# Kernel optimization log

Hardware: AMD Instinct MI355X
Metric: run time of the kernel (lower is better)

Reference implementation:

```python
import jax, jax.numpy as jnp
import numpy as np

B, N, START = 16, 16, 2048
D, H, HK, DH, CTX = 4096, 32, 8, 128, 4096
T = START + N
REP = H // HK
ROPE_THETA = 500000.0


def setup_inputs() -> dict:
    key = jax.random.key(0)
    ks = jax.random.split(key, 8)
    x = jax.random.normal(ks[0], (B, N, D), jnp.float32)
    # rotary frequencies for absolute positions START..T-1
    half = DH // 2
    inv_freq = 1.0 / (ROPE_THETA ** (np.arange(half, dtype=np.float64) * 2.0 / DH))
    pos = np.arange(START, T, dtype=np.float64)
    ang = pos[:, None] * inv_freq[None, :]  # (N, DH//2)
    freqs_cos = jnp.asarray(np.cos(ang), jnp.float32)
    freqs_sin = jnp.asarray(np.sin(ang), jnp.float32)
    # causal additive mask: query i (abs pos START+i) may attend to key j <= START+i
    i = np.arange(N)[:, None]
    j = np.arange(T)[None, :]
    mask = np.where(j <= START + i, 0.0, -1e9).astype(np.float32)
    mask = jnp.asarray(mask)[None, None]  # (1,1,N,T)
    cache_k = jax.random.normal(ks[1], (B, HK, CTX, DH), jnp.float32)
    cache_v = jax.random.normal(ks[2], (B, HK, CTX, DH), jnp.float32)
    s = 0.02
    wq = jax.random.normal(ks[3], (D, H * DH), jnp.float32) * s
    wk = jax.random.normal(ks[4], (D, HK * DH), jnp.float32) * s
    wv = jax.random.normal(ks[5], (D, HK * DH), jnp.float32) * s
    wo = jax.random.normal(ks[6], (D, D), jnp.float32) * s
    return {"x": x, "freqs_cos": freqs_cos, "freqs_sin": freqs_sin, "mask": mask,
            "cache_k": cache_k, "cache_v": cache_v,
            "wq": wq, "wk": wk, "wv": wv, "wo": wo, "start_pos": START}


def _rope(t, cos, sin):
    # t: (B, N, h, DH); cos/sin: (N, DH//2) -> broadcast (1, N, 1, DH//2)
    tr = t.reshape(*t.shape[:-1], -1, 2)
    a, b = tr[..., 0], tr[..., 1]
    c = cos[None, :, None, :]
    s = sin[None, :, None, :]
    out = jnp.stack([a * c - b * s, a * s + b * c], axis=-1)
    return out.reshape(t.shape)


def reference(x, freqs_cos, freqs_sin, mask, cache_k, cache_v, wq, wk, wv, wo, start_pos):
    Bx, Nx, _ = x.shape
    t_end = start_pos + Nx
    xq = (x @ wq).reshape(Bx, Nx, H, DH)
    xk = (x @ wk).reshape(Bx, Nx, HK, DH)
    xv = (x @ wv).reshape(Bx, Nx, HK, DH)
    xq = _rope(xq, freqs_cos, freqs_sin)
    xk = _rope(xk, freqs_cos, freqs_sin)
    xq = xq.transpose(0, 2, 1, 3)  # (B,H,N,DH)
    xk = xk.transpose(0, 2, 1, 3)  # (B,HK,N,DH)
    xv = xv.transpose(0, 2, 1, 3)
    # KV-cache scatter update, then slice to current length
    cache_k = cache_k.at[:, :, start_pos:t_end].set(xk)
    cache_v = cache_v.at[:, :, start_pos:t_end].set(xv)
    k = cache_k[:, :, :t_end]  # (B,HK,T,DH)
    v = cache_v[:, :, :t_end]
    # GQA masked SDPA
    q = xq.reshape(Bx, HK, REP, Nx, DH)
    scale = 1.0 / jnp.sqrt(jnp.float32(DH))
    scores = jnp.einsum('bkrnd,bktd->bkrnt', q, k) * scale
    scores = scores + mask[:, :, None]  # (1,1,1,N,T) broadcast
    p = jax.nn.softmax(scores, axis=-1)
    z = jnp.einsum('bkrnt,bktd->bkrnd', p, v)
    z = z.reshape(Bx, H, Nx, DH).transpose(0, 2, 1, 3).reshape(Bx, Nx, D)
    return z @ wo
```

## Files before the change

kernel.cpp:

```cpp
#include <hip/hip_runtime.h>


#define CTX 4096

typedef __attribute__((ext_vector_type(8))) short short8;
typedef __attribute__((ext_vector_type(4))) float f32x4;

__device__ __forceinline__ unsigned short f2bf(float f) {
  union { float f; unsigned u; } a; a.f = f;
  unsigned r = a.u + 0x7FFFu + ((a.u >> 16) & 1u);
  return (unsigned short)(r >> 16);
}

__device__ __forceinline__ f32x4 mfma_bf16(short8 a, short8 b, f32x4 c) {
  return __builtin_amdgcn_mfma_f32_16x16x32_bf16(a, b, c, 0, 0, 0);
}

__global__ __launch_bounds__(256) void k_cvt(const float* __restrict__ x,
                                             unsigned short* __restrict__ xb) {
  int e4 = blockIdx.x * 256 + threadIdx.x;
  float4 v = ((const float4*)x)[e4];
  ushort4 o; o.x = f2bf(v.x); o.y = f2bf(v.y); o.z = f2bf(v.z); o.w = f2bf(v.w);
  ((ushort4*)xb)[e4] = o;
}

struct SmemGemm {
  unsigned short As[128][72];
  unsigned short Bs[64][72];
};

__device__ __forceinline__ void gemm_body(SmemGemm& sm,
    const unsigned short* __restrict__ A, const float* __restrict__ B,
    float* __restrict__ C, int bm, int bn, int ldb, int ldc)
{
  const int tid = threadIdx.x;
  const int w = tid >> 6, lane = tid & 63, quad = lane >> 4, l16 = lane & 15;
  const int wm = (w & 1) << 6, wn = (w >> 1) << 5;

  const unsigned short* Ab = A + bm * 128 * 4096;
  const float* Bb = B + bn * 64;

  f32x4 acc[4][2];
#pragma unroll
  for (int mf = 0; mf < 4; ++mf)
#pragma unroll
    for (int nf = 0; nf < 2; ++nf) acc[mf][nf] = (f32x4){0.f, 0.f, 0.f, 0.f};

  uint4 pa[4]; float4 pb[4];

#define LOAD_TILES(KT_) do { \
    _Pragma("unroll") for (int i = 0; i < 4; ++i) { \
      int u = tid + (i << 8); \
      pa[i] = *(const uint4*)(Ab + (u >> 3) * 4096 + (KT_) * 64 + (u & 7) * 8); \
      pb[i] = *(const float4*)(Bb + (long)((KT_) * 64 + (u >> 4)) * ldb + (u & 15) * 4); \
    } } while (0)
#define STORE_TILES() do { \
    _Pragma("unroll") for (int i = 0; i < 4; ++i) { \
      int u = tid + (i << 8); \
      *(uint4*)&sm.As[u >> 3][(u & 7) * 8] = pa[i]; \
      const float* pf_ = (const float*)&pb[i]; \
      _Pragma("unroll") for (int c = 0; c < 4; ++c) \
        sm.Bs[(u & 15) * 4 + c][u >> 4] = f2bf(pf_[c]); \
    } } while (0)

  LOAD_TILES(0);
  STORE_TILES();
  __syncthreads();

  for (int kt = 0; kt < 64; ++kt) {
    if (kt < 63) LOAD_TILES(kt + 1);
#pragma unroll
    for (int kk = 0; kk < 2; ++kk) {
      short8 af[4], bfr[2];
#pragma unroll
      for (int mf = 0; mf < 4; ++mf)
        af[mf] = *(const short8*)&sm.As[wm + mf * 16 + l16][kk * 32 + quad * 8];
#pragma unroll
      for (int nf = 0; nf < 2; ++nf)
        bfr[nf] = *(const short8*)&sm.Bs[wn + nf * 16 + l16][kk * 32 + quad * 8];
#pragma unroll
      for (int mf = 0; mf < 4; ++mf)
#pragma unroll
        for (int nf = 0; nf < 2; ++nf)
          acc[mf][nf] = mfma_bf16(af[mf], bfr[nf], acc[mf][nf]);
    }
    __syncthreads();
    if (kt < 63) STORE_TILES();
    __syncthreads();
  }
#undef LOAD_TILES
#undef STORE_TILES

#pragma unroll
  for (int mf = 0; mf < 4; ++mf)
#pragma unroll
    for (int nf = 0; nf < 2; ++nf)
#pragma unroll
      for (int r = 0; r < 4; ++r)
        C[(long)(bm * 128 + wm + mf * 16 + quad * 4 + r) * ldc + bn * 64 + wn + nf * 16 + l16]
            = acc[mf][nf][r];
}

__global__ __launch_bounds__(256) void k_qkv(const unsigned short* __restrict__ xb,
    const float* __restrict__ wq, const float* __restrict__ wk, const float* __restrict__ wv,
    float* __restrict__ qb, float* __restrict__ kb, float* __restrict__ vb)
{
  __shared__ SmemGemm sm;
  int bn = blockIdx.x, bm = blockIdx.y;
  const float* B; float* C; int ldb, bnl;
  if (bn < 64)      { B = wq; C = qb; ldb = 4096; bnl = bn; }
  else if (bn < 80) { B = wk; C = kb; ldb = 1024; bnl = bn - 64; }
  else              { B = wv; C = vb; ldb = 1024; bnl = bn - 80; }
  gemm_body(sm, xb, B, C, bm, bnl, ldb, ldb);
}

__global__ __launch_bounds__(256) void k_oproj(const unsigned short* __restrict__ zb,
    const float* __restrict__ wo, float* __restrict__ out)
{
  __shared__ SmemGemm sm;
  gemm_body(sm, zb, wo, out, blockIdx.y, blockIdx.x, 4096, 4096);
}

__global__ __launch_bounds__(256) void k_kvfin(const float* __restrict__ kbuf,
    const float* __restrict__ vbuf, const float* __restrict__ fcos,
    const float* __restrict__ fsin, float* __restrict__ ck, float* __restrict__ cv)
{
  int id = blockIdx.x * 256 + threadIdx.x;
  if (id < 131072) {
    int m = id >> 9, pc = id & 511;
    int b = m >> 4, npos = m & 15;
    int hk = pc >> 6, fi = pc & 63;
    float a  = kbuf[m * 1024 + hk * 128 + 2 * fi];
    float b2 = kbuf[m * 1024 + hk * 128 + 2 * fi + 1];
    float c = fcos[npos * 64 + fi], s = fsin[npos * 64 + fi];
    float* dst = ck + ((size_t)(b * 8 + hk) * CTX + 2048 + npos) * 128 + 2 * fi;
    dst[0] = a * c - b2 * s;
    dst[1] = a * s + b2 * c;
  } else {
    int e = id - 131072;
    int m = e >> 10, cc = e & 1023;
    int b = m >> 4, npos = m & 15;
    int hk = cc >> 7, dh = cc & 127;
    cv[((size_t)(b * 8 + hk) * CTX + 2048 + npos) * 128 + dh] = vbuf[e];
  }
}

__global__ __launch_bounds__(256) void k_attn(const float* __restrict__ qb,
    const float* __restrict__ ck, const float* __restrict__ cv,
    const float* __restrict__ fcos, const float* __restrict__ fsin,
    float* __restrict__ zpO, float* __restrict__ zpL)
{
  __shared__ unsigned short Ks[32][136];
  __shared__ unsigned short Vs[128][40];
  __shared__ unsigned short Ps[4][16][40];

  const int tid = threadIdx.x;
  const int w = tid >> 6, lane = tid & 63, quad = lane >> 4, l16 = lane & 15;
  const int bid = blockIdx.x;
  const int half = bid & 1, hk = (bid >> 1) & 7, b = bid >> 4;
  const int h = hk * 4 + w;
  const float scale = 0.08838834764831845f;

  short8 qf[4];
  {
    const float* qrow = qb + (size_t)(b * 16 + l16) * 4096 + h * 128;
#pragma unroll
    for (int kf = 0; kf < 4; ++kf) {
      float t[8];
      *(float4*)&t[0] = *(const float4*)(qrow + kf * 32 + quad * 8);
      *(float4*)&t[4] = *(const float4*)(qrow + kf * 32 + quad * 8 + 4);
#pragma unroll
      for (int p = 0; p < 4; ++p) {
        int dh = kf * 32 + quad * 8 + 2 * p;
        int fi = dh >> 1;
        float c = fcos[l16 * 64 + fi], s = fsin[l16 * 64 + fi];
        float a = t[2 * p], b2 = t[2 * p + 1];
        qf[kf][2 * p]     = (short)f2bf((a * c - b2 * s) * scale);
        qf[kf][2 * p + 1] = (short)f2bf((a * s + b2 * c) * scale);
      }
    }
  }

  const float* Kg = ck + (size_t)(b * 8 + hk) * CTX * 128;
  const float* Vg = cv + (size_t)(b * 8 + hk) * CTX * 128;
  const int tb = half * 1024;
  const int NT = half ? 33 : 32;

  f32x4 O[8];
#pragma unroll
  for (int df = 0; df < 8; ++df) O[df] = (f32x4){0.f, 0.f, 0.f, 0.f};
  float lp[4] = {0.f, 0.f, 0.f, 0.f};

  float4 pk[4], pv[4];
#define A_LOAD(IT_) do { \
    _Pragma("unroll") for (int i = 0; i < 4; ++i) { \
      int u = tid + (i << 8); int trow = u >> 5, c4 = u & 31; \
      size_t off = (size_t)(tb + (IT_) * 32 + trow) * 128 + c4 * 4; \
      pk[i] = *(const float4*)(Kg + off); \
      pv[i] = *(const float4*)(Vg + off); \
    } } while (0)
#define A_STORE() do { \
    _Pragma("unroll") for (int i = 0; i < 4; ++i) { \
      int u = tid + (i << 8); int trow = u >> 5, c4 = u & 31; \
      ushort4 k4; k4.x = f2bf(pk[i].x); k4.y = f2bf(pk[i].y); \
      k4.z = f2bf(pk[i].z); k4.w = f2bf(pk[i].w); \
      *(ushort4*)&Ks[trow][c4 * 4] = k4; \
      Vs[c4 * 4 + 0][trow] = f2bf(pv[i].x); \
      Vs[c4 * 4 + 1][trow] = f2bf(pv[i].y); \
      Vs[c4 * 4 + 2][trow] = f2bf(pv[i].z); \
      Vs[c4 * 4 + 3][trow] = f2bf(pv[i].w); \
    } } while (0)

  A_LOAD(0);
  A_STORE();
  __syncthreads();

  for (int it = 0; it < NT; ++it) {
    if (it + 1 < NT) A_LOAD(it + 1);

    f32x4 S0 = (f32x4){0.f,0.f,0.f,0.f}, S1 = (f32x4){0.f,0.f,0.f,0.f};
#pragma unroll
    for (int kf = 0; kf < 4; ++kf) {
      short8 k0 = *(const short8*)&Ks[l16][kf * 32 + quad * 8];
      short8 k1 = *(const short8*)&Ks[16 + l16][kf * 32 + quad * 8];
      S0 = mfma_bf16(qf[kf], k0, S0);
      S1 = mfma_bf16(qf[kf], k1, S1);
    }

    const bool lastT = (half == 1) && (it == 32);
    float p0[4], p1[4];
#pragma unroll
    for (int r = 0; r < 4; ++r) {
      int row = quad * 4 + r;
      if (!lastT) { p0[r] = __expf(S0[r]); p1[r] = __expf(S1[r]); }
      else        { p0[r] = (l16 <= row) ? __expf(S0[r]) : 0.f; p1[r] = 0.f; }
      lp[r] += p0[r] + p1[r];
      Ps[w][row][l16]      = f2bf(p0[r]);
      Ps[w][row][16 + l16] = f2bf(p1[r]);
    }

    short8 pf = *(const short8*)&Ps[w][l16][quad * 8];
#pragma unroll
    for (int df = 0; df < 8; ++df) {
      short8 vb = *(const short8*)&Vs[df * 16 + l16][quad * 8];
      O[df] = mfma_bf16(pf, vb, O[df]);
    }

    __syncthreads();
    if (it + 1 < NT) A_STORE();
    __syncthreads();
  }
#undef A_LOAD
#undef A_STORE

#pragma unroll
  for (int r = 0; r < 4; ++r) {
#pragma unroll
    for (int off = 1; off < 16; off <<= 1) lp[r] += __shfl_xor(lp[r], off);
  }

#pragma unroll
  for (int df = 0; df < 8; ++df)
#pragma unroll
    for (int r = 0; r < 4; ++r)
      zpO[(size_t)(half * 256 + b * 16 + quad * 4 + r) * 4096 + h * 128 + df * 16 + l16]
          = O[df][r];

  if (l16 == 0) {
#pragma unroll
    for (int r = 0; r < 4; ++r)
      zpL[((half * 16 + b) * 32 + h) * 16 + quad * 4 + r] = lp[r];
  }
}

__global__ __launch_bounds__(256) void k_combine(const float* __restrict__ zpO,
    const float* __restrict__ zpL, unsigned short* __restrict__ zb)
{
  int e = blockIdx.x * 256 + threadIdx.x;
  int m = e >> 12, col = e & 4095;
  int b = m >> 4, npos = m & 15, h = col >> 7;
  float l0 = zpL[(b * 32 + h) * 16 + npos];
  float l1 = zpL[((16 + b) * 32 + h) * 16 + npos];
  float z = (zpO[e] + zpO[1048576 + e]) / (l0 + l1);
  zb[e] = f2bf(z);
}

extern "C" void kernel_launch(void* const* d_in, const int* in_sizes, int n_in,
                              void* d_out, int out_size, void* d_ws, size_t ws_size,
                              hipStream_t stream) {
  const float* x  = (const float*)d_in[0];
  const float* fc = (const float*)d_in[1];
  const float* fs = (const float*)d_in[2];
  float* ck = (float*)d_in[4];
  float* cv = (float*)d_in[5];
  const float* wq = (const float*)d_in[6];
  const float* wk = (const float*)d_in[7];
  const float* wv = (const float*)d_in[8];
  const float* wo = (const float*)d_in[9];
  float* out = (float*)d_out;

  char* ws = (char*)d_ws;
  unsigned short* xb = (unsigned short*)ws;
  float* qb   = (float*)(ws + (2u << 20));
  float* kbuf = (float*)(ws + (6u << 20));
  float* vbuf = (float*)(ws + (7u << 20));
  unsigned short* zb = (unsigned short*)(ws + (8u << 20));
  float* zpO  = (float*)(ws + (10u << 20));
  float* zpL  = (float*)(ws + (18u << 20));

  k_cvt<<<1024, 256, 0, stream>>>(x, xb);
  k_qkv<<<dim3(96, 2), 256, 0, stream>>>(xb, wq, wk, wv, qb, kbuf, vbuf);
  k_kvfin<<<1536, 256, 0, stream>>>(kbuf, vbuf, fc, fs, ck, cv);
  k_attn<<<256, 256, 0, stream>>>(qb, ck, cv, fc, fs, zpO, zpL);
  k_combine<<<4096, 256, 0, stream>>>(zpO, zpL, zb);
  k_oproj<<<dim3(64, 2), 256, 0, stream>>>(zb, wo, out);
}
```

Before: 752.4 us.

## Pre-transpose weights to bf16, split-K GEMMs with direct LDS loads, 4-way attention split

A new prep kernel converts and transposes all weight matrices to bf16 on every call. The GEMMs then stream both operands with global_load_lds into unpadded LDS tiles, and split K in two to double the block count. The partial sums are added in kvfin, in the attention Q load and in a new final add kernel. Attention splits the KV range four ways instead of two for more blocks. Together these aim to lift occupancy on the tiny M=256 GEMMs, at the cost of an extra full pass over roughly 100MB of fp32 weights, more partial-sum traffic and possible LDS bank conflicts from the unpadded layout.

```diff
diff --git a/kernel.cpp b/kernel.cpp
--- a/kernel.cpp
+++ b/kernel.cpp
@@ -16,29 +16,67 @@
   return __builtin_amdgcn_mfma_f32_16x16x32_bf16(a, b, c, 0, 0, 0);
 }
 
-__global__ __launch_bounds__(256) void k_cvt(const float* __restrict__ x,
-                                             unsigned short* __restrict__ xb) {
-  int e4 = blockIdx.x * 256 + threadIdx.x;
-  float4 v = ((const float4*)x)[e4];
-  ushort4 o; o.x = f2bf(v.x); o.y = f2bf(v.y); o.z = f2bf(v.z); o.w = f2bf(v.w);
-  ((ushort4*)xb)[e4] = o;
-}
-
-struct SmemGemm {
-  unsigned short As[128][72];
-  unsigned short Bs[64][72];
-};
-
-__device__ __forceinline__ void gemm_body(SmemGemm& sm,
-    const unsigned short* __restrict__ A, const float* __restrict__ B,
-    float* __restrict__ C, int bm, int bn, int ldb, int ldc)
-{
+__device__ __forceinline__ void gll16(const unsigned short* g, unsigned short* l) {
+  __builtin_amdgcn_global_load_lds(
+      (__attribute__((address_space(1))) unsigned int*)(g),
+      (__attribute__((address_space(3))) unsigned int*)(l), 16, 0, 0);
+}
+
+__global__ __launch_bounds__(256) void k_prep(const float* __restrict__ wq,
+    const float* __restrict__ wk, const float* __restrict__ wv,
+    const float* __restrict__ wo, const float* __restrict__ x,
+    unsigned short* __restrict__ wqkvT, unsigned short* __restrict__ woT,
+    unsigned short* __restrict__ xb)
+{
+  const int bid = blockIdx.x, tid = threadIdx.x;
+  if (bid >= 10240) {
+    int e4 = (bid - 10240) * 256 + tid;
+    float4 v = ((const float4*)x)[e4];
+    ushort4 o; o.x = f2bf(v.x); o.y = f2bf(v.y); o.z = f2bf(v.z); o.w = f2bf(v.w);
+    ((ushort4*)xb)[e4] = o;
+    return;
+  }
+  __shared__ unsigned short Ts[64][66];
+  const float* src; unsigned short* dst; int N; int t = bid;
+  if (t < 4096)      {            src = wq; dst = wqkvT;                        N = 4096; }
+  else if (t < 5120) { t -= 4096; src = wk; dst = wqkvT + (size_t)4096 * 4096;  N = 1024; }
+  else if (t < 6144) { t -= 5120; src = wv; dst = wqkvT + (size_t)5120 * 4096;  N = 1024; }
+  else               { t -= 6144; src = wo; dst = woT;                          N = 4096; }
+  const int kt = t & 63, bn = t >> 6;
+  const int k0 = kt * 64, n0 = bn * 64;
+#pragma unroll
+  for (int i = 0; i < 4; ++i) {
+    int u = tid + i * 256;
+    int k = u >> 4, n4 = u & 15;
+    float4 v = *(const float4*)(src + (size_t)(k0 + k) * N + n0 + n4 * 4);
+    Ts[k][n4 * 4 + 0] = f2bf(v.x); Ts[k][n4 * 4 + 1] = f2bf(v.y);
+    Ts[k][n4 * 4 + 2] = f2bf(v.z); Ts[k][n4 * 4 + 3] = f2bf(v.w);
+  }
+  __syncthreads();
+#pragma unroll
+  for (int i = 0; i < 2; ++i) {
+    int u = tid + i * 256;
+    int nn = u >> 3, cc = u & 7;
+    unsigned short v[8];
+#pragma unroll
+    for (int j = 0; j < 8; ++j) v[j] = Ts[cc * 8 + j][nn];
+    *(short8*)(dst + (size_t)(n0 + nn) * 4096 + k0 + cc * 8) = *(const short8*)v;
+  }
+}
+
+__global__ __launch_bounds__(256) void k_gemm(const unsigned short* __restrict__ A,
+    const unsigned short* __restrict__ BT, float* __restrict__ Cp, int Ntot)
+{
+  __shared__ unsigned short sA[128 * 64];
+  __shared__ unsigned short sB[64 * 64];
   const int tid = threadIdx.x;
   const int w = tid >> 6, lane = tid & 63, quad = lane >> 4, l16 = lane & 15;
   const int wm = (w & 1) << 6, wn = (w >> 1) << 5;
-
-  const unsigned short* Ab = A + bm * 128 * 4096;
-  const float* Bb = B + bn * 64;
+  const int bn = blockIdx.x, bm = blockIdx.y, ks = blockIdx.z;
+  const int r8 = lane >> 3, c8 = (lane & 7) << 3;
+
+  const unsigned short* Ab = A + (size_t)(bm * 128) * 4096 + (ks << 11);
+  const unsigned short* Bb = BT + (size_t)(bn * 64) * 4096 + (ks << 11);
 
   f32x4 acc[4][2];
 #pragma unroll
@@ -46,38 +84,25 @@
 #pragma unroll
     for (int nf = 0; nf < 2; ++nf) acc[mf][nf] = (f32x4){0.f, 0.f, 0.f, 0.f};
 
-  uint4 pa[4]; float4 pb[4];
-
-#define LOAD_TILES(KT_) do { \
-    _Pragma("unroll") for (int i = 0; i < 4; ++i) { \
-      int u = tid + (i << 8); \
-      pa[i] = *(const uint4*)(Ab + (u >> 3) * 4096 + (KT_) * 64 + (u & 7) * 8); \
-      pb[i] = *(const float4*)(Bb + (long)((KT_) * 64 + (u >> 4)) * ldb + (u & 15) * 4); \
-    } } while (0)
-#define STORE_TILES() do { \
-    _Pragma("unroll") for (int i = 0; i < 4; ++i) { \
-      int u = tid + (i << 8); \
-      *(uint4*)&sm.As[u >> 3][(u & 7) * 8] = pa[i]; \
-      const float* pf_ = (const float*)&pb[i]; \
-      _Pragma("unroll") for (int c = 0; c < 4; ++c) \
-        sm.Bs[(u & 15) * 4 + c][u >> 4] = f2bf(pf_[c]); \
-    } } while (0)
-
-  LOAD_TILES(0);
-  STORE_TILES();
-  __syncthreads();
-
-  for (int kt = 0; kt < 64; ++kt) {
-    if (kt < 63) LOAD_TILES(kt + 1);
+  for (int kt = 0; kt < 32; ++kt) {
+#pragma unroll
+    for (int i = 0; i < 4; ++i)
+      gll16(Ab + (size_t)(w * 32 + i * 8 + r8) * 4096 + kt * 64 + c8,
+            &sA[(w * 32 + i * 8) * 64]);
+#pragma unroll
+    for (int i = 0; i < 2; ++i)
+      gll16(Bb + (size_t)(w * 16 + i * 8 + r8) * 4096 + kt * 64 + c8,
+            &sB[(w * 16 + i * 8) * 64]);
+    __syncthreads();
 #pragma unroll
     for (int kk = 0; kk < 2; ++kk) {
       short8 af[4], bfr[2];
 #pragma unroll
       for (int mf = 0; mf < 4; ++mf)
-        af[mf] = *(const short8*)&sm.As[wm + mf * 16 + l16][kk * 32 + quad * 8];
+        af[mf] = *(const short8*)&sA[(wm + mf * 16 + l16) * 64 + kk * 32 + quad * 8];
 #pragma unroll
       for (int nf = 0; nf < 2; ++nf)
-        bfr[nf] = *(const short8*)&sm.Bs[wn + nf * 16 + l16][kk * 32 + quad * 8];
+        bfr[nf] = *(const short8*)&sB[(wn + nf * 16 + l16) * 64 + kk * 32 + quad * 8];
 #pragma unroll
       for (int mf = 0; mf < 4; ++mf)
 #pragma unroll
@@ -85,53 +110,32 @@
           acc[mf][nf] = mfma_bf16(af[mf], bfr[nf], acc[mf][nf]);
     }
     __syncthreads();
-    if (kt < 63) STORE_TILES();
-    __syncthreads();
-  }
-#undef LOAD_TILES
-#undef STORE_TILES
-
+  }
+
+  float* Cz = Cp + (size_t)ks * 256 * Ntot;
 #pragma unroll
   for (int mf = 0; mf < 4; ++mf)
 #pragma unroll
     for (int nf = 0; nf < 2; ++nf)
 #pragma unroll
       for (int r = 0; r < 4; ++r)
-        C[(long)(bm * 128 + wm + mf * 16 + quad * 4 + r) * ldc + bn * 64 + wn + nf * 16 + l16]
-            = acc[mf][nf][r];
-}
-
-__global__ __launch_bounds__(256) void k_qkv(const unsigned short* __restrict__ xb,
-    const float* __restrict__ wq, const float* __restrict__ wk, const float* __restrict__ wv,
-    float* __restrict__ qb, float* __restrict__ kb, float* __restrict__ vb)
-{
-  __shared__ SmemGemm sm;
-  int bn = blockIdx.x, bm = blockIdx.y;
-  const float* B; float* C; int ldb, bnl;
-  if (bn < 64)      { B = wq; C = qb; ldb = 4096; bnl = bn; }
-  else if (bn < 80) { B = wk; C = kb; ldb = 1024; bnl = bn - 64; }
-  else              { B = wv; C = vb; ldb = 1024; bnl = bn - 80; }
-  gemm_body(sm, xb, B, C, bm, bnl, ldb, ldb);
-}
-
-__global__ __launch_bounds__(256) void k_oproj(const unsigned short* __restrict__ zb,
-    const float* __restrict__ wo, float* __restrict__ out)
-{
-  __shared__ SmemGemm sm;
-  gemm_body(sm, zb, wo, out, blockIdx.y, blockIdx.x, 4096, 4096);
-}
-
-__global__ __launch_bounds__(256) void k_kvfin(const float* __restrict__ kbuf,
-    const float* __restrict__ vbuf, const float* __restrict__ fcos,
-    const float* __restrict__ fsin, float* __restrict__ ck, float* __restrict__ cv)
-{
+        Cz[(size_t)(bm * 128 + wm + mf * 16 + quad * 4 + r) * Ntot
+           + bn * 64 + wn + nf * 16 + l16] = acc[mf][nf][r];
+}
+
+__global__ __launch_bounds__(256) void k_kvfin(const float* __restrict__ qp,
+    const float* __restrict__ fcos, const float* __restrict__ fsin,
+    float* __restrict__ ck, float* __restrict__ cv)
+{
+  const float* qp1 = qp + (size_t)256 * 6144;
   int id = blockIdx.x * 256 + threadIdx.x;
   if (id < 131072) {
     int m = id >> 9, pc = id & 511;
     int b = m >> 4, npos = m & 15;
     int hk = pc >> 6, fi = pc & 63;
-    float a  = kbuf[m * 1024 + hk * 128 + 2 * fi];
-    float b2 = kbuf[m * 1024 + hk * 128 + 2 * fi + 1];
+    size_t off = (size_t)m * 6144 + 4096 + hk * 128 + 2 * fi;
+    float a  = qp[off] + qp1[off];
+    float b2 = qp[off + 1] + qp1[off + 1];
     float c = fcos[npos * 64 + fi], s = fsin[npos * 64 + fi];
     float* dst = ck + ((size_t)(b * 8 + hk) * CTX + 2048 + npos) * 128 + 2 * fi;
     dst[0] = a * c - b2 * s;
@@ -141,11 +145,12 @@
     int m = e >> 10, cc = e & 1023;
     int b = m >> 4, npos = m & 15;
     int hk = cc >> 7, dh = cc & 127;
-    cv[((size_t)(b * 8 + hk) * CTX + 2048 + npos) * 128 + dh] = vbuf[e];
-  }
-}
-
-__global__ __launch_bounds__(256) void k_attn(const float* __restrict__ qb,
+    size_t off = (size_t)m * 6144 + 5120 + cc;
+    cv[((size_t)(b * 8 + hk) * CTX + 2048 + npos) * 128 + dh] = qp[off] + qp1[off];
+  }
+}
+
+__global__ __launch_bounds__(256) void k_attn(const float* __restrict__ qp,
     const float* __restrict__ ck, const float* __restrict__ cv,
     const float* __restrict__ fcos, const float* __restrict__ fsin,
     float* __restrict__ zpO, float* __restrict__ zpL)
@@ -157,18 +162,23 @@
   const int tid = threadIdx.x;
   const int w = tid >> 6, lane = tid & 63, quad = lane >> 4, l16 = lane & 15;
   const int bid = blockIdx.x;
-  const int half = bid & 1, hk = (bid >> 1) & 7, b = bid >> 4;
+  const int split = bid & 3, hk = (bid >> 2) & 7, b = bid >> 5;
   const int h = hk * 4 + w;
   const float scale = 0.08838834764831845f;
 
   short8 qf[4];
   {
-    const float* qrow = qb + (size_t)(b * 16 + l16) * 4096 + h * 128;
+    const float* q0 = qp + (size_t)(b * 16 + l16) * 6144 + h * 128;
+    const float* q1 = q0 + (size_t)256 * 6144;
 #pragma unroll
     for (int kf = 0; kf < 4; ++kf) {
       float t[8];
-      *(float4*)&t[0] = *(const float4*)(qrow + kf * 32 + quad * 8);
-      *(float4*)&t[4] = *(const float4*)(qrow + kf * 32 + quad * 8 + 4);
+#pragma unroll
+      for (int j = 0; j < 4; ++j) {
+        int o = kf * 32 + quad * 8 + j;
+        t[j]     = q0[o] + q1[o];
+        t[4 + j] = q0[o + 4] + q1[o + 4];
+      }
 #pragma unroll
       for (int p = 0; p < 4; ++p) {
         int dh = kf * 32 + quad * 8 + 2 * p;
@@ -183,8 +193,8 @@
 
   const float* Kg = ck + (size_t)(b * 8 + hk) * CTX * 128;
   const float* Vg = cv + (size_t)(b * 8 + hk) * CTX * 128;
-  const int tb = half * 1024;
-  const int NT = half ? 33 : 32;
+  const int tb = split * 512;
+  const int NT = (split == 3) ? 17 : 16;
 
   f32x4 O[8];
 #pragma unroll
@@ -227,7 +237,7 @@
       S1 = mfma_bf16(qf[kf], k1, S1);
     }
 
-    const bool lastT = (half == 1) && (it == 32);
+    const bool lastT = (split == 3) && (it == 16);
     float p0[4], p1[4];
 #pragma unroll
     for (int r = 0; r < 4; ++r) {
@@ -254,22 +264,21 @@
 #undef A_STORE
 
 #pragma unroll
-  for (int r = 0; r < 4; ++r) {
+  for (int r = 0; r < 4; ++r)
 #pragma unroll
     for (int off = 1; off < 16; off <<= 1) lp[r] += __shfl_xor(lp[r], off);
-  }
 
 #pragma unroll
   for (int df = 0; df < 8; ++df)
 #pragma unroll
     for (int r = 0; r < 4; ++r)
-      zpO[(size_t)(half * 256 + b * 16 + quad * 4 + r) * 4096 + h * 128 + df * 16 + l16]
+      zpO[(size_t)(split * 256 + b * 16 + quad * 4 + r) * 4096 + h * 128 + df * 16 + l16]
           = O[df][r];
 
   if (l16 == 0) {
 #pragma unroll
     for (int r = 0; r < 4; ++r)
-      zpL[((half * 16 + b) * 32 + h) * 16 + quad * 4 + r] = lp[r];
+      zpL[((split * 16 + b) * 32 + h) * 16 + quad * 4 + r] = lp[r];
   }
 }
 
@@ -279,10 +288,23 @@
   int e = blockIdx.x * 256 + threadIdx.x;
   int m = e >> 12, col = e & 4095;
   int b = m >> 4, npos = m & 15, h = col >> 7;
-  float l0 = zpL[(b * 32 + h) * 16 + npos];
-  float l1 = zpL[((16 + b) * 32 + h) * 16 + npos];
-  float z = (zpO[e] + zpO[1048576 + e]) / (l0 + l1);
-  zb[e] = f2bf(z);
+  float num = 0.f, den = 0.f;
+#pragma unroll
+  for (int s = 0; s < 4; ++s) {
+    num += zpO[(size_t)s * 1048576 + e];
+    den += zpL[((s * 16 + b) * 32 + h) * 16 + npos];
+  }
+  zb[e] = f2bf(num / den);
+}
+
+__global__ __launch_bounds__(256) void k_fin(const float* __restrict__ op,
+                                             float* __restrict__ out)
+{
+  int e4 = blockIdx.x * 256 + threadIdx.x;
+  float4 a = ((const float4*)op)[e4];
+  float4 b = ((const float4*)(op + (size_t)1048576))[e4];
+  float4 o; o.x = a.x + b.x; o.y = a.y + b.y; o.z = a.z + b.z; o.w = a.w + b.w;
+  ((float4*)out)[e4] = o;
 }
 
 extern "C" void kernel_launch(void* const* d_in, const int* in_sizes, int n_in,
@@ -300,18 +322,22 @@
   float* out = (float*)d_out;
 
   char* ws = (char*)d_ws;
-  unsigned short* xb = (unsigned short*)ws;
-  float* qb   = (float*)(ws + (2u << 20));
-  float* kbuf = (float*)(ws + (6u << 20));
-  float* vbuf = (float*)(ws + (7u << 20));
-  unsigned short* zb = (unsigned short*)(ws + (8u << 20));
-  float* zpO  = (float*)(ws + (10u << 20));
-  float* zpL  = (float*)(ws + (18u << 20));
-
-  k_cvt<<<1024, 256, 0, stream>>>(x, xb);
-  k_qkv<<<dim3(96, 2), 256, 0, stream>>>(xb, wq, wk, wv, qb, kbuf, vbuf);
-  k_kvfin<<<1536, 256, 0, stream>>>(kbuf, vbuf, fc, fs, ck, cv);
-  k_attn<<<256, 256, 0, stream>>>(qb, ck, cv, fc, fs, zpO, zpL);
+#define MB(x) ((size_t)(x) << 20)
+  unsigned short* xb    = (unsigned short*)(ws);
+  unsigned short* wqkvT = (unsigned short*)(ws + MB(2));
+  unsigned short* woT   = (unsigned short*)(ws + MB(50));
+  float*          qpart = (float*)(ws + MB(82));
+  unsigned short* zb    = (unsigned short*)(ws + MB(95));
+  float*          zpO   = (float*)(ws + MB(97));
+  float*          zpL   = (float*)(ws + MB(113));
+  float*          opart = (float*)(ws + MB(114));
+#undef MB
+
+  k_prep<<<11264, 256, 0, stream>>>(wq, wk, wv, wo, x, wqkvT, woT, xb);
+  k_gemm<<<dim3(96, 2, 2), 256, 0, stream>>>(xb, wqkvT, qpart, 6144);
+  k_kvfin<<<1536, 256, 0, stream>>>(qpart, fc, fs, ck, cv);
+  k_attn<<<512, 256, 0, stream>>>(qpart, ck, cv, fc, fs, zpO, zpL);
   k_combine<<<4096, 256, 0, stream>>>(zpO, zpL, zb);
-  k_oproj<<<dim3(64, 2), 256, 0, stream>>>(zb, wo, out);
-}
+  k_gemm<<<dim3(64, 2, 2), 256, 0, stream>>>(zb, woT, opart, 4096);
+  k_fin<<<1024, 256, 0, stream>>>(opart, out);
+}
```

After: 675.5 us. -10.2%, faster.
